# Kernel tuning notes

Hardware: AMD Instinct MI355X
Metric: run time of the kernel (lower is better)

The kernel has to match this reference:

```python
import jax, jax.numpy as jnp
import numpy as np

BASE_TEMP = 0.07
CLASS_TEMPS = jnp.array([0.08, 0.05, 0.10], dtype=jnp.float32)  # idx 0,1,2
EPS = 1e-08


def setup_inputs() -> dict:
    key = jax.random.key(0)
    k1, k2 = jax.random.split(key)
    B, D = 8192, 128
    embeddings = jax.random.normal(k1, (B, D), dtype=jnp.float32)
    labels = jax.random.randint(k2, (B,), 0, 3, dtype=jnp.int64)
    return {"embeddings": embeddings, "labels": labels}


def reference(embeddings, labels):
    B = embeddings.shape[0]
    # per-row temperature from the row's class label
    temps = CLASS_TEMPS[labels]  # [B]
    sim = jnp.matmul(embeddings, embeddings.T)  # [B, B]
    logits = sim / temps[:, None]
    # subtract detached row max (stability, gradient-stopped as in .detach())
    logits = logits - jax.lax.stop_gradient(jnp.max(logits, axis=1, keepdims=True))
    # denominator includes the self term (original sums exp over all j)
    log_prob = logits - jnp.log(jnp.sum(jnp.exp(logits), axis=1, keepdims=True) + EPS)
    # positives: same label, excluding self
    pos_mask = (labels[:, None] == labels[None, :]).astype(jnp.float32)
    pos_mask = pos_mask * (1.0 - jnp.eye(B, dtype=jnp.float32))
    pos_count = jnp.sum(pos_mask, axis=1)  # [B]
    valid = pos_count > 0
    loss_i = -(BASE_TEMP / temps) * jnp.sum(pos_mask * log_prob, axis=1) / (pos_count + EPS)
    n_valid = jnp.sum(valid.astype(jnp.float32))
    total = jnp.sum(jnp.where(valid, loss_i, 0.0))
    return jnp.where(n_valid > 0, total / jnp.maximum(n_valid, 1.0), 0.0)
```

## Files before the change

### kernel.cpp

```cpp
#include <hip/hip_runtime.h>
#include <hip/hip_bf16.h>


#define B_ROWS 8192
#define D_DIM 128
#define NSPLIT 16
#define JRANGE (B_ROWS / NSPLIT)
#define NSTEPS (JRANGE / 32)
#define BASE_TEMP 0.07f
#define LOG2E 1.4426950408889634f
#define LN2 0.6931471805599453f
#define FIX_SCALE 1048576.0f

typedef __bf16 bf16x8 __attribute__((ext_vector_type(8)));
typedef __bf16 bf16x4 __attribute__((ext_vector_type(4)));
typedef float floatx16 __attribute__((ext_vector_type(16)));
typedef unsigned long long u64;

__device__ __forceinline__ float class_invtemp(int lbl) {
    return (lbl == 0) ? 12.5f : ((lbl == 1) ? 20.0f : 10.0f);
}

__device__ __forceinline__ u64 fix64(float v) {
    return (u64)(long long)llrintf(v * FIX_SCALE);
}

__global__ __launch_bounds__(256) void k0_prep(
        const float* __restrict__ E, const int* __restrict__ labels,
        __bf16* __restrict__ Ebf, __bf16* __restrict__ Ebs,
        float* __restrict__ nrm,
        float* __restrict__ Spart ,
        int* __restrict__ cntpart ) {
    const int blk = blockIdx.x;
    const int tid = threadIdx.x;
    const int row0 = blk * 32;

    __shared__ float sh[3][128];
    __shared__ int scnt[3];
    if (tid < 3) scnt[tid] = 0;

    const float4* src = reinterpret_cast<const float4*>(E + (size_t)row0 * D_DIM);
    #pragma unroll
    for (int p = 0; p < 4; ++p) {
        int idx = p * 256 + tid;
        float4 v = src[idx];
        int r = idx >> 5, k4 = idx & 31;
        int R = row0 + r;
        float sc = class_invtemp(labels[R]) * LOG2E;
        int T = R >> 5;
        int l = (R & 31) + ((k4 >> 1) & 1) * 32;
        int c = k4 >> 2;
        size_t dst = (size_t)T * 4096 + c * 512 + l * 8 + (k4 & 1) * 4;
        bf16x4 o  = { (__bf16)v.x, (__bf16)v.y, (__bf16)v.z, (__bf16)v.w };
        bf16x4 os = { (__bf16)(v.x * sc), (__bf16)(v.y * sc),
                      (__bf16)(v.z * sc), (__bf16)(v.w * sc) };
        *reinterpret_cast<bf16x4*>(Ebf + dst) = o;
        *reinterpret_cast<bf16x4*>(Ebs + dst) = os;
        float s = v.x * v.x + v.y * v.y + v.z * v.z + v.w * v.w;
        s += __shfl_xor(s, 1);  s += __shfl_xor(s, 2);  s += __shfl_xor(s, 4);
        s += __shfl_xor(s, 8);  s += __shfl_xor(s, 16);
        if ((tid & 31) == 0) nrm[R] = s;
    }

    const int d = tid & 127, half = tid >> 7;
    float s0 = 0.f, s1 = 0.f, s2 = 0.f;
    #pragma unroll 4
    for (int r2 = 0; r2 < 16; ++r2) {
        int r = row0 + half * 16 + r2;
        float v = E[(size_t)r * D_DIM + d];
        int l = labels[r];
        s0 += (l == 0) ? v : 0.f;
        s1 += (l == 1) ? v : 0.f;
        s2 += (l == 2) ? v : 0.f;
    }
    if (half == 1) { sh[0][d] = s0; sh[1][d] = s1; sh[2][d] = s2; }
    if (tid < 32) atomicAdd(&scnt[labels[row0 + tid]], 1);
    __syncthreads();
    if (half == 0) {
        Spart[((size_t)blk * 3 + 0) * 128 + d] = s0 + sh[0][d];
        Spart[((size_t)blk * 3 + 1) * 128 + d] = s1 + sh[1][d];
        Spart[((size_t)blk * 3 + 2) * 128 + d] = s2 + sh[2][d];
    }
    if (tid < 3) cntpart[blk * 4 + tid] = scnt[tid];
}

__global__ __launch_bounds__(256, 2) void k2_stats(
        const __bf16* __restrict__ Ebf, const __bf16* __restrict__ Ebs,
        const int* __restrict__ labels, const float* __restrict__ nrm,
        float* __restrict__ part ,
        const float* __restrict__ Spart, const int* __restrict__ cntpart,
        float* __restrict__ S , float* __restrict__ counts ,
        u64* __restrict__ lossfix, u64* __restrict__ validfix,
        unsigned int* __restrict__ done) {
    __shared__ __bf16 Ab[2][4096];

    const int tid = threadIdx.x;
    const int lane = tid & 63;
    const int wave = tid >> 6;
    const int itile = blockIdx.x;
    const int split = blockIdx.y;
    const int col = lane & 31;
    const int icol0 = itile * 256 + wave * 64 + col;
    const int icol1 = icol0 + 32;

    const float negm0 = -class_invtemp(labels[icol0]) * LOG2E * nrm[icol0];
    const float negm1 = -class_invtemp(labels[icol1]) * LOG2E * nrm[icol1];

    const int iT0 = itile * 8 + wave * 2;
    const __bf16* b0 = Ebs + (size_t)iT0 * 4096 + lane * 8;
    bf16x8 Bf0[8], Bf1[8];
    #pragma unroll
    for (int c = 0; c < 8; ++c) {
        Bf0[c] = *reinterpret_cast<const bf16x8*>(b0 + c * 512);
        Bf1[c] = *reinterpret_cast<const bf16x8*>(b0 + 4096 + c * 512);
    }

    const __bf16* abase = Ebf + (size_t)split * NSTEPS * 4096;

    {
        const float4* s0 = reinterpret_cast<const float4*>(abase);
        float4* d0 = reinterpret_cast<float4*>(&Ab[0][0]);
        d0[tid] = s0[tid];
        d0[tid + 256] = s0[tid + 256];
    }
    __syncthreads();

    float Zacc0[4], Zacc1[4];
    #pragma unroll
    for (int q = 0; q < 4; ++q) { Zacc0[q] = 0.f; Zacc1[q] = 0.f; }

    for (int s = 0; s < NSTEPS; ++s) {
        float4 nxt0, nxt1;
        if (s + 1 < NSTEPS) {
            const float4* sp = reinterpret_cast<const float4*>(
                abase + (size_t)(s + 1) * 4096);
            nxt0 = sp[tid];
            nxt1 = sp[tid + 256];
        }

        const __bf16* abuf = &Ab[s & 1][0];
        bf16x8 A[8];
        #pragma unroll
        for (int c = 0; c < 8; ++c)
            A[c] = *reinterpret_cast<const bf16x8*>(abuf + c * 512 + lane * 8);

        floatx16 a0, a1;
        #pragma unroll
        for (int r = 0; r < 16; ++r) { a0[r] = negm0; a1[r] = negm1; }
        #pragma unroll
        for (int c = 0; c < 8; ++c) {
            a0 = __builtin_amdgcn_mfma_f32_32x32x16_bf16(A[c], Bf0[c], a0, 0, 0, 0);
            a1 = __builtin_amdgcn_mfma_f32_32x32x16_bf16(A[c], Bf1[c], a1, 0, 0, 0);
        }

        #pragma unroll
        for (int q = 0; q < 4; ++q) {
            Zacc0[q] += (__builtin_amdgcn_exp2f(a0[4 * q])
                       + __builtin_amdgcn_exp2f(a0[4 * q + 1]))
                      + (__builtin_amdgcn_exp2f(a0[4 * q + 2])
                       + __builtin_amdgcn_exp2f(a0[4 * q + 3]));
            Zacc1[q] += (__builtin_amdgcn_exp2f(a1[4 * q])
                       + __builtin_amdgcn_exp2f(a1[4 * q + 1]))
                      + (__builtin_amdgcn_exp2f(a1[4 * q + 2])
                       + __builtin_amdgcn_exp2f(a1[4 * q + 3]));
        }

        if (s + 1 < NSTEPS) {
            float4* dn = reinterpret_cast<float4*>(&Ab[(s + 1) & 1][0]);
            dn[tid] = nxt0;
            dn[tid + 256] = nxt1;
        }
        __syncthreads();
    }

    float Zt0 = (Zacc0[0] + Zacc0[1]) + (Zacc0[2] + Zacc0[3]);
    float Zt1 = (Zacc1[0] + Zacc1[1]) + (Zacc1[2] + Zacc1[3]);
    Zt0 += __shfl_xor(Zt0, 32);
    Zt1 += __shfl_xor(Zt1, 32);
    if (lane < 32) {
        part[(size_t)split * B_ROWS + icol0] = Zt0;
        part[(size_t)split * B_ROWS + icol1] = Zt1;
    }

    if (split == 0) {
        if (itile < 3 && tid < 128) {
            float a = 0.f;
            #pragma unroll 8
            for (int g = 0; g < 256; ++g)
                a += Spart[((size_t)g * 3 + itile) * 128 + tid];
            S[itile * 128 + tid] = a;
        } else if (itile == 3 && tid < 3) {
            int a = 0;
            #pragma unroll 8
            for (int g = 0; g < 256; ++g) a += cntpart[g * 4 + tid];
            counts[tid] = (float)a;
        } else if (itile == 4 && tid == 0) {
            *lossfix = 0ull;
            *validfix = 0ull;
            *done = 0u;
        }
    }
}

__global__ __launch_bounds__(256) void k3_rowloss(
        const float* __restrict__ E, const int* __restrict__ labels,
        const float* __restrict__ S, const float* __restrict__ counts,
        const float* __restrict__ nrm, const float* __restrict__ part,
        u64* __restrict__ lossfix, u64* __restrict__ validfix,
        unsigned int* __restrict__ done, float* __restrict__ out) {
    __shared__ float sS[384];
    const int tid = threadIdx.x;
    if (tid < 128) {
        sS[tid]       = S[tid];
        sS[128 + tid] = S[128 + tid];
        sS[256 + tid] = S[256 + tid];
    }
    __syncthreads();

    const int r = tid >> 3, g = tid & 7;
    const int i = blockIdx.x * 32 + r;
    const int lab = labels[i];
    const float invt = class_invtemp(lab);

    const float4* er = reinterpret_cast<const float4*>(E + (size_t)i * D_DIM);
    const float4* sr = reinterpret_cast<const float4*>(&sS[lab * 128]);
    float dotS = 0.f;
    #pragma unroll
    for (int q = 0; q < 4; ++q) {
        float4 v = er[g * 4 + q];
        float4 s = sr[g * 4 + q];
        dotS += v.x * s.x + v.y * s.y + v.z * s.z + v.w * s.w;
    }
    float Zp = 0.f;
    #pragma unroll
    for (int p = 0; p < NSPLIT / 8; ++p)
        Zp += part[(size_t)(g + p * 8) * B_ROWS + i];

    #pragma unroll
    for (int off = 1; off < 8; off <<= 1) {
        dotS += __shfl_xor(dotS, off);
        Zp   += __shfl_xor(Zp, off);
    }

    float loss = 0.f;
    int valid = 0;
    if (g == 0) {
        const float nr = nrm[i];
        const float C = counts[lab] - 1.0f;
        const float lse = invt * nr + LN2 * __builtin_amdgcn_logf(Zp);
        const float P_nat = invt * (dotS - nr);
        if (C > 0.f) {
            loss = -(BASE_TEMP * invt) * (P_nat - C * lse) / (C + 1e-8f);
            valid = 1;
        }
    }
    loss += __shfl_down(loss, 8);   valid += __shfl_down(valid, 8);
    loss += __shfl_down(loss, 16);  valid += __shfl_down(valid, 16);
    loss += __shfl_down(loss, 32);  valid += __shfl_down(valid, 32);

    __shared__ float rl[4];
    __shared__ int rv[4];
    if ((tid & 63) == 0) { rl[tid >> 6] = loss; rv[tid >> 6] = valid; }
    __syncthreads();
    if (tid == 0) {
        float bt = (rl[0] + rl[1]) + (rl[2] + rl[3]);
        int bv = (rv[0] + rv[1]) + (rv[2] + rv[3]);
        atomicAdd(lossfix, fix64(bt));
        atomicAdd(validfix, (u64)bv);
        __threadfence();
        unsigned int t = atomicAdd(done, 1u);
        if (t == gridDim.x - 1) {
            u64 L = atomicAdd(lossfix, 0ull);
            u64 V = atomicAdd(validfix, 0ull);
            double T = (double)(long long)L * (1.0 / (double)FIX_SCALE);
            double N = (double)(long long)V;
            out[0] = (N > 0.0) ? (float)(T / fmax(N, 1.0)) : 0.f;
        }
    }
}

extern "C" void kernel_launch(void* const* d_in, const int* in_sizes, int n_in,
                              void* d_out, int out_size, void* d_ws, size_t ws_size,
                              hipStream_t stream) {
    const float* E = (const float*)d_in[0];
    const int* labels = (const int*)d_in[1];
    float* out = (float*)d_out;
    char* ws = (char*)d_ws;

    const size_t OFF_EBF   = 0;
    const size_t OFF_EBS   = (size_t)2 << 20;
    const size_t OFF_NRM   = (size_t)4 << 20;
    const size_t OFF_SPART = OFF_NRM + 32768;
    const size_t OFF_CNTP  = OFF_SPART + 393216;
    const size_t OFF_S     = OFF_CNTP + 4096;
    const size_t OFF_MISC  = OFF_S + 2048;
    const size_t OFF_PART  = OFF_MISC + 256;

    __bf16* Ebf = (__bf16*)(ws + OFF_EBF);
    __bf16* Ebs = (__bf16*)(ws + OFF_EBS);
    float* nrm = (float*)(ws + OFF_NRM);
    float* Spart = (float*)(ws + OFF_SPART);
    int* cntpart = (int*)(ws + OFF_CNTP);
    float* S = (float*)(ws + OFF_S);
    float* counts = (float*)(ws + OFF_MISC);
    u64* lossfix = (u64*)(ws + OFF_MISC + 16);
    u64* validfix = (u64*)(ws + OFF_MISC + 24);
    unsigned int* done = (unsigned int*)(ws + OFF_MISC + 32);
    float* part = (float*)(ws + OFF_PART);

    k0_prep<<<256, 256, 0, stream>>>(E, labels, Ebf, Ebs, nrm, Spart, cntpart);
    k2_stats<<<dim3(32, NSPLIT), 256, 0, stream>>>(
        Ebf, Ebs, labels, nrm, part, Spart, cntpart, S, counts,
        lossfix, validfix, done);
    k3_rowloss<<<256, 256, 0, stream>>>(E, labels, S, counts, nrm, part,
                                        lossfix, validfix, done, out);
}
```

Measured before the change: 48.46 us.

## Drop LDS staging in stats kernel, software-pipeline MFMA and exp, double splits

The stats kernel no longer stages A tiles through shared memory with barriers. Each lane now loads its A fragments straight from global memory into registers, double-buffered, and the loop is fully unrolled so one step's MFMA chain overlaps the previous step's exp2 reductions. NSPLIT goes from 16 to 32 to launch more blocks, and the prep kernel computes per-class sums from the already-loaded float4 values instead of re-reading E. The part buffer is moved to a fixed offset to fit the larger split. Trade-offs are higher register pressure, redundant global or L2 loads across waves, and more partial sums for the later kernel to combine.

```diff
diff --git a/kernel.cpp b/kernel.cpp
--- a/kernel.cpp
+++ b/kernel.cpp
@@ -4,7 +4,7 @@
 
 #define B_ROWS 8192
 #define D_DIM 128
-#define NSPLIT 16
+#define NSPLIT 32
 #define JRANGE (B_ROWS / NSPLIT)
 #define NSTEPS (JRANGE / 32)
 #define BASE_TEMP 0.07f
@@ -35,9 +35,13 @@
     const int tid = threadIdx.x;
     const int row0 = blk * 32;
 
-    __shared__ float sh[3][128];
+    __shared__ float4 red[3][256];
     __shared__ int scnt[3];
     if (tid < 3) scnt[tid] = 0;
+
+    float4 cls0 = {0.f, 0.f, 0.f, 0.f};
+    float4 cls1 = {0.f, 0.f, 0.f, 0.f};
+    float4 cls2 = {0.f, 0.f, 0.f, 0.f};
 
     const float4* src = reinterpret_cast<const float4*>(E + (size_t)row0 * D_DIM);
     #pragma unroll
@@ -46,7 +50,8 @@
         float4 v = src[idx];
         int r = idx >> 5, k4 = idx & 31;
         int R = row0 + r;
-        float sc = class_invtemp(labels[R]) * LOG2E;
+        int lab = labels[R];
+        float sc = class_invtemp(lab) * LOG2E;
         int T = R >> 5;
         int l = (R & 31) + ((k4 >> 1) & 1) * 32;
         int c = k4 >> 2;
@@ -60,26 +65,27 @@
         s += __shfl_xor(s, 1);  s += __shfl_xor(s, 2);  s += __shfl_xor(s, 4);
         s += __shfl_xor(s, 8);  s += __shfl_xor(s, 16);
         if ((tid & 31) == 0) nrm[R] = s;
-    }
-
-    const int d = tid & 127, half = tid >> 7;
-    float s0 = 0.f, s1 = 0.f, s2 = 0.f;
-    #pragma unroll 4
-    for (int r2 = 0; r2 < 16; ++r2) {
-        int r = row0 + half * 16 + r2;
-        float v = E[(size_t)r * D_DIM + d];
-        int l = labels[r];
-        s0 += (l == 0) ? v : 0.f;
-        s1 += (l == 1) ? v : 0.f;
-        s2 += (l == 2) ? v : 0.f;
-    }
-    if (half == 1) { sh[0][d] = s0; sh[1][d] = s1; sh[2][d] = s2; }
+        if (lab == 0) { cls0.x += v.x; cls0.y += v.y; cls0.z += v.z; cls0.w += v.w; }
+        else if (lab == 1) { cls1.x += v.x; cls1.y += v.y; cls1.z += v.z; cls1.w += v.w; }
+        else { cls2.x += v.x; cls2.y += v.y; cls2.z += v.z; cls2.w += v.w; }
+    }
+    red[0][tid] = cls0;
+    red[1][tid] = cls1;
+    red[2][tid] = cls2;
     if (tid < 32) atomicAdd(&scnt[labels[row0 + tid]], 1);
     __syncthreads();
-    if (half == 0) {
-        Spart[((size_t)blk * 3 + 0) * 128 + d] = s0 + sh[0][d];
-        Spart[((size_t)blk * 3 + 1) * 128 + d] = s1 + sh[1][d];
-        Spart[((size_t)blk * 3 + 2) * 128 + d] = s2 + sh[2][d];
+
+    if (tid < 128) {
+        const int k4 = tid >> 2, comp = tid & 3;
+        const float* rf = reinterpret_cast<const float*>(red);
+        #pragma unroll
+        for (int c = 0; c < 3; ++c) {
+            float a = 0.f;
+            #pragma unroll
+            for (int w = 0; w < 8; ++w)
+                a += rf[(c * 256 + k4 + 32 * w) * 4 + comp];
+            Spart[((size_t)blk * 3 + c) * 128 + tid] = a;
+        }
     }
     if (tid < 3) cntpart[blk * 4 + tid] = scnt[tid];
 }
@@ -92,8 +98,6 @@
         float* __restrict__ S , float* __restrict__ counts ,
         u64* __restrict__ lossfix, u64* __restrict__ validfix,
         unsigned int* __restrict__ done) {
-    __shared__ __bf16 Ab[2][4096];
-
     const int tid = threadIdx.x;
     const int lane = tid & 63;
     const int wave = tid >> 6;
@@ -115,63 +119,68 @@
         Bf1[c] = *reinterpret_cast<const bf16x8*>(b0 + 4096 + c * 512);
     }
 
-    const __bf16* abase = Ebf + (size_t)split * NSTEPS * 4096;
-
-    {
-        const float4* s0 = reinterpret_cast<const float4*>(abase);
-        float4* d0 = reinterpret_cast<float4*>(&Ab[0][0]);
-        d0[tid] = s0[tid];
-        d0[tid + 256] = s0[tid + 256];
-    }
-    __syncthreads();
+    const __bf16* abase = Ebf + (size_t)split * NSTEPS * 4096 + lane * 8;
+    bf16x8 A0[8], A1[8];
+    #pragma unroll
+    for (int c = 0; c < 8; ++c)
+        A0[c] = *reinterpret_cast<const bf16x8*>(abase + c * 512);
 
     float Zacc0[4], Zacc1[4];
     #pragma unroll
     for (int q = 0; q < 4; ++q) { Zacc0[q] = 0.f; Zacc1[q] = 0.f; }
 
-    for (int s = 0; s < NSTEPS; ++s) {
-        float4 nxt0, nxt1;
-        if (s + 1 < NSTEPS) {
-            const float4* sp = reinterpret_cast<const float4*>(
-                abase + (size_t)(s + 1) * 4096);
-            nxt0 = sp[tid];
-            nxt1 = sp[tid + 256];
-        }
-
-        const __bf16* abuf = &Ab[s & 1][0];
-        bf16x8 A[8];
-        #pragma unroll
-        for (int c = 0; c < 8; ++c)
-            A[c] = *reinterpret_cast<const bf16x8*>(abuf + c * 512 + lane * 8);
-
-        floatx16 a0, a1;
-        #pragma unroll
-        for (int r = 0; r < 16; ++r) { a0[r] = negm0; a1[r] = negm1; }
-        #pragma unroll
-        for (int c = 0; c < 8; ++c) {
-            a0 = __builtin_amdgcn_mfma_f32_32x32x16_bf16(A[c], Bf0[c], a0, 0, 0, 0);
-            a1 = __builtin_amdgcn_mfma_f32_32x32x16_bf16(A[c], Bf1[c], a1, 0, 0, 0);
-        }
-
-        #pragma unroll
-        for (int q = 0; q < 4; ++q) {
-            Zacc0[q] += (__builtin_amdgcn_exp2f(a0[4 * q])
-                       + __builtin_amdgcn_exp2f(a0[4 * q + 1]))
-                      + (__builtin_amdgcn_exp2f(a0[4 * q + 2])
-                       + __builtin_amdgcn_exp2f(a0[4 * q + 3]));
-            Zacc1[q] += (__builtin_amdgcn_exp2f(a1[4 * q])
-                       + __builtin_amdgcn_exp2f(a1[4 * q + 1]))
-                      + (__builtin_amdgcn_exp2f(a1[4 * q + 2])
-                       + __builtin_amdgcn_exp2f(a1[4 * q + 3]));
-        }
-
-        if (s + 1 < NSTEPS) {
-            float4* dn = reinterpret_cast<float4*>(&Ab[(s + 1) & 1][0]);
-            dn[tid] = nxt0;
-            dn[tid + 256] = nxt1;
-        }
-        __syncthreads();
-    }
+    floatx16 ea0, ea1, oa0, oa1;
+
+#define CHAIN(dst0, dst1, Ab)                                                  \
+    {                                                                          \
+        _Pragma("unroll")                                                      \
+        for (int r = 0; r < 16; ++r) { dst0[r] = negm0; dst1[r] = negm1; }     \
+        _Pragma("unroll")                                                      \
+        for (int c = 0; c < 8; ++c) {                                          \
+            dst0 = __builtin_amdgcn_mfma_f32_32x32x16_bf16(Ab[c], Bf0[c], dst0, 0, 0, 0); \
+            dst1 = __builtin_amdgcn_mfma_f32_32x32x16_bf16(Ab[c], Bf1[c], dst1, 0, 0, 0); \
+        }                                                                      \
+    }
+
+#define EXPSTEP(src0, src1)                                                    \
+    {                                                                          \
+        _Pragma("unroll")                                                      \
+        for (int q = 0; q < 4; ++q) {                                          \
+            Zacc0[q] += (__builtin_amdgcn_exp2f(src0[4 * q])                   \
+                       + __builtin_amdgcn_exp2f(src0[4 * q + 1]))              \
+                      + (__builtin_amdgcn_exp2f(src0[4 * q + 2])               \
+                       + __builtin_amdgcn_exp2f(src0[4 * q + 3]));             \
+            Zacc1[q] += (__builtin_amdgcn_exp2f(src1[4 * q])                   \
+                       + __builtin_amdgcn_exp2f(src1[4 * q + 1]))              \
+                      + (__builtin_amdgcn_exp2f(src1[4 * q + 2])               \
+                       + __builtin_amdgcn_exp2f(src1[4 * q + 3]));             \
+        }                                                                      \
+    }
+
+    #pragma unroll
+    for (int s = 0; s < NSTEPS; s += 2) {
+        {
+            const __bf16* ap = abase + (size_t)(s + 1) * 4096;
+            #pragma unroll
+            for (int c = 0; c < 8; ++c)
+                A1[c] = *reinterpret_cast<const bf16x8*>(ap + c * 512);
+            CHAIN(ea0, ea1, A0)
+            if (s > 0) EXPSTEP(oa0, oa1)
+        }
+        {
+            if (s + 2 < NSTEPS) {
+                const __bf16* ap = abase + (size_t)(s + 2) * 4096;
+                #pragma unroll
+                for (int c = 0; c < 8; ++c)
+                    A0[c] = *reinterpret_cast<const bf16x8*>(ap + c * 512);
+            }
+            CHAIN(oa0, oa1, A1)
+            EXPSTEP(ea0, ea1)
+        }
+    }
+    EXPSTEP(oa0, oa1)
+#undef CHAIN
+#undef EXPSTEP
 
     float Zt0 = (Zacc0[0] + Zacc0[1]) + (Zacc0[2] + Zacc0[3]);
     float Zt1 = (Zacc1[0] + Zacc1[1]) + (Zacc1[2] + Zacc1[3]);
@@ -294,7 +303,7 @@
     const size_t OFF_CNTP  = OFF_SPART + 393216;
     const size_t OFF_S     = OFF_CNTP + 4096;
     const size_t OFF_MISC  = OFF_S + 2048;
-    const size_t OFF_PART  = OFF_MISC + 256;
+    const size_t OFF_PART  = (size_t)5 << 20;
 
     __bf16* Ebf = (__bf16*)(ws + OFF_EBF);
     __bf16* Ebs = (__bf16*)(ws + OFF_EBS);
```

Result: slower. 72.31 us (+49.2%).

## Halve per-wave column tile in stats kernel and fuse class sums into prep loop

Applied to the files above, without the earlier changes.

The stats kernel now gives each wave one 32-column tile instead of two, and splits the K dimension across two independent MFMA accumulator chains that are summed before exp2. Twice as many blocks are launched, and the launch-bounds occupancy hint is dropped. This cuts register pressure and shortens the dependent MFMA chains, but A-tile LDS traffic doubles per output. Separately, the prep kernel accumulates the per-class sums from values it has already loaded instead of re-reading E, then reduces them through shared memory.

```diff
diff --git a/kernel.cpp b/kernel.cpp
--- a/kernel.cpp
+++ b/kernel.cpp
@@ -35,9 +35,13 @@
     const int tid = threadIdx.x;
     const int row0 = blk * 32;
 
-    __shared__ float sh[3][128];
+    __shared__ float4 red[3][256];
     __shared__ int scnt[3];
     if (tid < 3) scnt[tid] = 0;
+
+    float4 cls0 = {0.f, 0.f, 0.f, 0.f};
+    float4 cls1 = {0.f, 0.f, 0.f, 0.f};
+    float4 cls2 = {0.f, 0.f, 0.f, 0.f};
 
     const float4* src = reinterpret_cast<const float4*>(E + (size_t)row0 * D_DIM);
     #pragma unroll
@@ -46,7 +50,8 @@
         float4 v = src[idx];
         int r = idx >> 5, k4 = idx & 31;
         int R = row0 + r;
-        float sc = class_invtemp(labels[R]) * LOG2E;
+        int lab = labels[R];
+        float sc = class_invtemp(lab) * LOG2E;
         int T = R >> 5;
         int l = (R & 31) + ((k4 >> 1) & 1) * 32;
         int c = k4 >> 2;
@@ -60,31 +65,32 @@
         s += __shfl_xor(s, 1);  s += __shfl_xor(s, 2);  s += __shfl_xor(s, 4);
         s += __shfl_xor(s, 8);  s += __shfl_xor(s, 16);
         if ((tid & 31) == 0) nrm[R] = s;
-    }
-
-    const int d = tid & 127, half = tid >> 7;
-    float s0 = 0.f, s1 = 0.f, s2 = 0.f;
-    #pragma unroll 4
-    for (int r2 = 0; r2 < 16; ++r2) {
-        int r = row0 + half * 16 + r2;
-        float v = E[(size_t)r * D_DIM + d];
-        int l = labels[r];
-        s0 += (l == 0) ? v : 0.f;
-        s1 += (l == 1) ? v : 0.f;
-        s2 += (l == 2) ? v : 0.f;
-    }
-    if (half == 1) { sh[0][d] = s0; sh[1][d] = s1; sh[2][d] = s2; }
+        if (lab == 0) { cls0.x += v.x; cls0.y += v.y; cls0.z += v.z; cls0.w += v.w; }
+        else if (lab == 1) { cls1.x += v.x; cls1.y += v.y; cls1.z += v.z; cls1.w += v.w; }
+        else { cls2.x += v.x; cls2.y += v.y; cls2.z += v.z; cls2.w += v.w; }
+    }
+    red[0][tid] = cls0;
+    red[1][tid] = cls1;
+    red[2][tid] = cls2;
     if (tid < 32) atomicAdd(&scnt[labels[row0 + tid]], 1);
     __syncthreads();
-    if (half == 0) {
-        Spart[((size_t)blk * 3 + 0) * 128 + d] = s0 + sh[0][d];
-        Spart[((size_t)blk * 3 + 1) * 128 + d] = s1 + sh[1][d];
-        Spart[((size_t)blk * 3 + 2) * 128 + d] = s2 + sh[2][d];
+
+    if (tid < 128) {
+        const int k4 = tid >> 2, comp = tid & 3;
+        const float* rf = reinterpret_cast<const float*>(red);
+        #pragma unroll
+        for (int c = 0; c < 3; ++c) {
+            float a = 0.f;
+            #pragma unroll
+            for (int w = 0; w < 8; ++w)
+                a += rf[(c * 256 + k4 + 32 * w) * 4 + comp];
+            Spart[((size_t)blk * 3 + c) * 128 + tid] = a;
+        }
     }
     if (tid < 3) cntpart[blk * 4 + tid] = scnt[tid];
 }
 
-__global__ __launch_bounds__(256, 2) void k2_stats(
+__global__ __launch_bounds__(256) void k2_stats(
         const __bf16* __restrict__ Ebf, const __bf16* __restrict__ Ebs,
         const int* __restrict__ labels, const float* __restrict__ nrm,
         float* __restrict__ part ,
@@ -100,20 +106,20 @@
     const int itile = blockIdx.x;
     const int split = blockIdx.y;
     const int col = lane & 31;
-    const int icol0 = itile * 256 + wave * 64 + col;
-    const int icol1 = icol0 + 32;
-
-    const float negm0 = -class_invtemp(labels[icol0]) * LOG2E * nrm[icol0];
-    const float negm1 = -class_invtemp(labels[icol1]) * LOG2E * nrm[icol1];
-
-    const int iT0 = itile * 8 + wave * 2;
-    const __bf16* b0 = Ebs + (size_t)iT0 * 4096 + lane * 8;
-    bf16x8 Bf0[8], Bf1[8];
-    #pragma unroll
-    for (int c = 0; c < 8; ++c) {
-        Bf0[c] = *reinterpret_cast<const bf16x8*>(b0 + c * 512);
-        Bf1[c] = *reinterpret_cast<const bf16x8*>(b0 + 4096 + c * 512);
-    }
+    const int icol = itile * 128 + wave * 32 + col;
+
+    const float negm = -class_invtemp(labels[icol]) * LOG2E * nrm[icol];
+
+    const int iT = itile * 4 + wave;
+    const __bf16* bbase = Ebs + (size_t)iT * 4096 + lane * 8;
+    bf16x8 Bf[8];
+    #pragma unroll
+    for (int c = 0; c < 8; ++c)
+        Bf[c] = *reinterpret_cast<const bf16x8*>(bbase + c * 512);
+
+    floatx16 init0;
+    #pragma unroll
+    for (int r = 0; r < 16; ++r) init0[r] = negm;
 
     const __bf16* abase = Ebf + (size_t)split * NSTEPS * 4096;
 
@@ -125,9 +131,9 @@
     }
     __syncthreads();
 
-    float Zacc0[4], Zacc1[4];
-    #pragma unroll
-    for (int q = 0; q < 4; ++q) { Zacc0[q] = 0.f; Zacc1[q] = 0.f; }
+    float Zacc[4];
+    #pragma unroll
+    for (int q = 0; q < 4; ++q) Zacc[q] = 0.f;
 
     for (int s = 0; s < NSTEPS; ++s) {
         float4 nxt0, nxt1;
@@ -144,25 +150,24 @@
         for (int c = 0; c < 8; ++c)
             A[c] = *reinterpret_cast<const bf16x8*>(abuf + c * 512 + lane * 8);
 
-        floatx16 a0, a1;
+        floatx16 a1;
         #pragma unroll
-        for (int r = 0; r < 16; ++r) { a0[r] = negm0; a1[r] = negm1; }
-        #pragma unroll
-        for (int c = 0; c < 8; ++c) {
-            a0 = __builtin_amdgcn_mfma_f32_32x32x16_bf16(A[c], Bf0[c], a0, 0, 0, 0);
-            a1 = __builtin_amdgcn_mfma_f32_32x32x16_bf16(A[c], Bf1[c], a1, 0, 0, 0);
-        }
+        for (int r = 0; r < 16; ++r) a1[r] = 0.f;
+        floatx16 a0 = __builtin_amdgcn_mfma_f32_32x32x16_bf16(A[0], Bf[0], init0, 0, 0, 0);
+        a1 = __builtin_amdgcn_mfma_f32_32x32x16_bf16(A[4], Bf[4], a1, 0, 0, 0);
+        a0 = __builtin_amdgcn_mfma_f32_32x32x16_bf16(A[1], Bf[1], a0, 0, 0, 0);
+        a1 = __builtin_amdgcn_mfma_f32_32x32x16_bf16(A[5], Bf[5], a1, 0, 0, 0);
+        a0 = __builtin_amdgcn_mfma_f32_32x32x16_bf16(A[2], Bf[2], a0, 0, 0, 0);
+        a1 = __builtin_amdgcn_mfma_f32_32x32x16_bf16(A[6], Bf[6], a1, 0, 0, 0);
+        a0 = __builtin_amdgcn_mfma_f32_32x32x16_bf16(A[3], Bf[3], a0, 0, 0, 0);
+        a1 = __builtin_amdgcn_mfma_f32_32x32x16_bf16(A[7], Bf[7], a1, 0, 0, 0);
 
         #pragma unroll
         for (int q = 0; q < 4; ++q) {
-            Zacc0[q] += (__builtin_amdgcn_exp2f(a0[4 * q])
-                       + __builtin_amdgcn_exp2f(a0[4 * q + 1]))
-                      + (__builtin_amdgcn_exp2f(a0[4 * q + 2])
-                       + __builtin_amdgcn_exp2f(a0[4 * q + 3]));
-            Zacc1[q] += (__builtin_amdgcn_exp2f(a1[4 * q])
-                       + __builtin_amdgcn_exp2f(a1[4 * q + 1]))
-                      + (__builtin_amdgcn_exp2f(a1[4 * q + 2])
-                       + __builtin_amdgcn_exp2f(a1[4 * q + 3]));
+            Zacc[q] += (__builtin_amdgcn_exp2f(a0[4 * q]     + a1[4 * q])
+                      + __builtin_amdgcn_exp2f(a0[4 * q + 1] + a1[4 * q + 1]))
+                     + (__builtin_amdgcn_exp2f(a0[4 * q + 2] + a1[4 * q + 2])
+                      + __builtin_amdgcn_exp2f(a0[4 * q + 3] + a1[4 * q + 3]));
         }
 
         if (s + 1 < NSTEPS) {
@@ -173,14 +178,10 @@
         __syncthreads();
     }
 
-    float Zt0 = (Zacc0[0] + Zacc0[1]) + (Zacc0[2] + Zacc0[3]);
-    float Zt1 = (Zacc1[0] + Zacc1[1]) + (Zacc1[2] + Zacc1[3]);
-    Zt0 += __shfl_xor(Zt0, 32);
-    Zt1 += __shfl_xor(Zt1, 32);
-    if (lane < 32) {
-        part[(size_t)split * B_ROWS + icol0] = Zt0;
-        part[(size_t)split * B_ROWS + icol1] = Zt1;
-    }
+    float Zt = (Zacc[0] + Zacc[1]) + (Zacc[2] + Zacc[3]);
+    Zt += __shfl_xor(Zt, 32);
+    if (lane < 32)
+        part[(size_t)split * B_ROWS + icol] = Zt;
 
     if (split == 0) {
         if (itile < 3 && tid < 128) {
@@ -294,7 +295,7 @@
     const size_t OFF_CNTP  = OFF_SPART + 393216;
     const size_t OFF_S     = OFF_CNTP + 4096;
     const size_t OFF_MISC  = OFF_S + 2048;
-    const size_t OFF_PART  = OFF_MISC + 256;
+    const size_t OFF_PART  = (size_t)5 << 20;
 
     __bf16* Ebf = (__bf16*)(ws + OFF_EBF);
     __bf16* Ebs = (__bf16*)(ws + OFF_EBS);
@@ -309,7 +310,7 @@
     float* part = (float*)(ws + OFF_PART);
 
     k0_prep<<<256, 256, 0, stream>>>(E, labels, Ebf, Ebs, nrm, Spart, cntpart);
-    k2_stats<<<dim3(32, NSPLIT), 256, 0, stream>>>(
+    k2_stats<<<dim3(64, NSPLIT), 256, 0, stream>>>(
         Ebf, Ebs, labels, nrm, part, Spart, cntpart, S, counts,
         lossfix, validfix, done);
     k3_rowloss<<<256, 256, 0, stream>>>(E, labels, S, counts, nrm, part,
```

After: 49.27 us. Within noise of the previous version (+1.7%).
